# Optimization experiments

Measured on AMD Instinct MI355X. Metric: run time of the kernel, lower is better.

Reference implementation:

```python
import jax, jax.numpy as jnp
import numpy as np

D_MODEL = 768
D_FF = 3072
N_EXPERTS = 4
BATCH, SEQ = 8, 2048


def setup_inputs() -> dict:
    key = jax.random.key(0)
    ks = jax.random.split(key, 8)
    s_in = 1.0 / np.sqrt(D_MODEL)
    s_ff = 1.0 / np.sqrt(D_FF)
    return {
        "hidden_states": jax.random.normal(ks[0], (BATCH, SEQ, D_MODEL), jnp.float32),
        "Wg": jax.random.normal(ks[1], (D_MODEL, N_EXPERTS), jnp.float32) * s_in,
        "bg": jnp.zeros((N_EXPERTS,), jnp.float32),
        "W1": jax.random.normal(ks[2], (N_EXPERTS, D_MODEL, D_FF), jnp.float32) * s_in,
        "b1": jnp.zeros((N_EXPERTS, D_FF), jnp.float32),
        "W2": jax.random.normal(ks[3], (N_EXPERTS, D_FF, D_MODEL), jnp.float32) * s_ff,
        "b2": jnp.zeros((N_EXPERTS, D_MODEL), jnp.float32),
    }


def reference(hidden_states, Wg, bg, W1, b1, W2, b2):
    """Switch-Transformer top-1 MoE FFN (no token dropping).

    router: softmax(x @ Wg + bg); each token goes to argmax expert,
    expert FFN: gelu(x @ W1[e] + b1[e]) @ W2[e] + b2[e],
    output scaled by the winning route probability.
    """
    B, S, D = hidden_states.shape
    xt = hidden_states.reshape(-1, D)                      # [T, D]
    logits = xt @ Wg + bg                                  # [T, E]
    probs = jax.nn.softmax(logits, axis=-1)
    gate = jnp.max(probs, axis=-1)                         # [T]
    route = jnp.argmax(probs, axis=-1)                     # [T] int

    out = jnp.zeros_like(xt)
    for e in range(W1.shape[0]):                           # small fixed expert count
        mask = (route == e).astype(xt.dtype)[:, None]      # [T, 1]
        h = jax.nn.gelu(xt @ W1[e] + b1[e])                # [T, d_ff]
        y = h @ W2[e] + b2[e]                              # [T, D]
        out = out + mask * y
    out = out * gate[:, None]
    return out.reshape(B, S, D)
```

## Files before the change

### kernel.cpp

```cpp
#include <hip/hip_runtime.h>
#include <hip/hip_bf16.h>

#define T_TOK 16384
#define DMODEL 768
#define DFF 3072
#define NEXP 4
#define ROWPAD 512
#define BK 64
#define MBLK_MAX (T_TOK / 128 + NEXP)

typedef __attribute__((ext_vector_type(8))) short bf16x8;
typedef __attribute__((ext_vector_type(4))) float f32x4;

__device__ __forceinline__ void gl_lds16(const void* g, void* l) {
  __builtin_amdgcn_global_load_lds(
      (const __attribute__((address_space(1))) unsigned int*)g,
      (__attribute__((address_space(3))) unsigned int*)l, 16, 0, 0);
}

__device__ __forceinline__ short f2bf(float f) {
  union { float f; unsigned u; } v; v.f = f;
  unsigned r = v.u + 0x7fff + ((v.u >> 16) & 1);
  return (short)(r >> 16);
}

__device__ __forceinline__ float gelu_f(float x) {
  const float c = 0.7978845608028654f;
  float z = c * (x + 0.044715f * x * x * x);
  z = fminf(fmaxf(z, -15.f), 15.f);
  float e = __expf(-2.f * z);
  return 0.5f * x * (1.f + (1.f - e) / (1.f + e));
}


__device__ __forceinline__ int expert_aoff(const int* counts, int e) {
  int off = 0;
  for (int i = 0; i < e; ++i) off += (counts[i] + 127) & ~127;
  return off;
}

__global__ void route_kernel(const float* __restrict__ x, const float* __restrict__ Wg,
                             const float* __restrict__ bg, int* __restrict__ route,
                             float* __restrict__ gate) {
  int t = blockIdx.x * 4 + (threadIdx.x >> 6);
  int l = threadIdx.x & 63;
  const float* xr = x + (size_t)t * DMODEL;
  float s0 = 0.f, s1 = 0.f, s2 = 0.f, s3 = 0.f;
#pragma unroll
  for (int i = 0; i < DMODEL / 64; ++i) {
    int d = l + i * 64;
    float xv = xr[d];
    float4 w = *((const float4*)Wg + d);
    s0 += xv * w.x; s1 += xv * w.y; s2 += xv * w.z; s3 += xv * w.w;
  }
#pragma unroll
  for (int off = 32; off; off >>= 1) {
    s0 += __shfl_xor(s0, off);
    s1 += __shfl_xor(s1, off);
    s2 += __shfl_xor(s2, off);
    s3 += __shfl_xor(s3, off);
  }
  if (l == 0) {
    float lg[4] = { s0 + bg[0], s1 + bg[1], s2 + bg[2], s3 + bg[3] };
    int best = 0; float m = lg[0];
#pragma unroll
    for (int e = 1; e < 4; ++e) if (lg[e] > m) { m = lg[e]; best = e; }
    float s = 0.f;
#pragma unroll
    for (int e = 0; e < 4; ++e) s += __expf(lg[e] - m);
    route[t] = best;
    gate[t] = 1.0f / s;
  }
}

__global__ void bucket_kernel(const int* __restrict__ route, int* __restrict__ counts,
                              int* __restrict__ perm) {
  __shared__ int wcnt[4][NEXP];
  __shared__ int wpre[4][NEXP];
  __shared__ int base[NEXP];
  int tid = threadIdx.x;
  int t = blockIdx.x * 256 + tid;
  int w = tid >> 6, l = tid & 63;
  int r = route[t];
  int lanepre = 0;
  unsigned long long lower = (l == 0) ? 0ull : (~0ull >> (64 - l));
#pragma unroll
  for (int e = 0; e < NEXP; ++e) {
    unsigned long long m = __ballot(r == e);
    if (l == 0) wcnt[w][e] = (int)__popcll(m);
    if (r == e) lanepre = (int)__popcll(m & lower);
  }
  __syncthreads();
  if (tid < NEXP) {
    int s = 0;
#pragma unroll
    for (int ww = 0; ww < 4; ++ww) { wpre[ww][tid] = s; s += wcnt[ww][tid]; }
    base[tid] = atomicAdd(&counts[tid], s);
  }
  __syncthreads();
  int pos = base[r] + wpre[w][r] + lanepre;
  perm[r * T_TOK + pos] = t;
}

__global__ void gather_kernel(const float* __restrict__ x, const int* __restrict__ counts,
                              const int* __restrict__ perm, const float* __restrict__ gate,
                              short* __restrict__ xg, int* __restrict__ tokg,
                              float* __restrict__ gateg) {
  int e = blockIdx.y;
  int cnt = counts[e];
  int pos = blockIdx.x * 8 + (threadIdx.x >> 5);
  if (pos >= cnt) return;
  int off = expert_aoff(counts, e);
  int t = perm[e * T_TOK + pos];
  int g = off + pos;
  int l = threadIdx.x & 31;
  const float* src = x + (size_t)t * DMODEL;
  short* dst = xg + (size_t)g * DMODEL;
  int sw = g & 7;
#pragma unroll
  for (int i = 0; i < 3; ++i) {
    int c = l + 32 * i;
    float4 a = *((const float4*)src + c * 2);
    float4 b = *((const float4*)src + c * 2 + 1);
    bf16x8 v;
    v[0] = f2bf(a.x); v[1] = f2bf(a.y); v[2] = f2bf(a.z); v[3] = f2bf(a.w);
    v[4] = f2bf(b.x); v[5] = f2bf(b.y); v[6] = f2bf(b.z); v[7] = f2bf(b.w);
    int cs = (c & ~7) | ((c & 7) ^ sw);
    *(bf16x8*)(dst + cs * 8) = v;
  }
  if (l == 0) { tokg[g] = t; gateg[g] = gate[t]; }
}

__global__ void transpose_kernel(const float* __restrict__ src, short* __restrict__ dst,
                                 int K, int N) {
  __shared__ float lds[64 * 65];
  int e = blockIdx.z;
  int k0 = blockIdx.x * 64, n0 = blockIdx.y * 64;
  const float* s = src + (size_t)e * K * N;
  short* d = dst + (size_t)e * N * K;
#pragma unroll
  for (int i = 0; i < 16; ++i) {
    int idx = threadIdx.x + i * 256;
    int kk = idx >> 6, nn = idx & 63;
    lds[kk * 65 + nn] = s[(size_t)(k0 + kk) * N + n0 + nn];
  }
  __syncthreads();
#pragma unroll
  for (int i = 0; i < 2; ++i) {
    int cid = threadIdx.x + i * 256;
    int nn = cid >> 3, uu = cid & 7;
    int n = n0 + nn;
    bf16x8 v;
#pragma unroll
    for (int j = 0; j < 8; ++j) v[j] = f2bf(lds[(uu * 8 + j) * 65 + nn]);
    int cs = (k0 >> 3) + (uu ^ (n & 7));
    *(bf16x8*)(d + (size_t)n * K + cs * 8) = v;
  }
}

__global__ void transpose_tiled_kernel(const float* __restrict__ src, short* __restrict__ dst,
                                       int K, int N) {
  __shared__ float lds[64 * 65];
  int e = blockIdx.z;
  int k0 = blockIdx.x * 64, n0 = blockIdx.y * 64;
  const float* s = src + (size_t)e * K * N;
#pragma unroll
  for (int i = 0; i < 16; ++i) {
    int idx = threadIdx.x + i * 256;
    int kk = idx >> 6, nn = idx & 63;
    lds[kk * 65 + nn] = s[(size_t)(k0 + kk) * N + n0 + nn];
  }
  __syncthreads();
  size_t tile = ((size_t)e * (K >> 6) + (k0 >> 6)) * (N >> 6) + (n0 >> 6);
  short* d = dst + tile * 4096;
#pragma unroll
  for (int i = 0; i < 2; ++i) {
    int cid = threadIdx.x + i * 256;
    int nn = cid >> 3, uu = cid & 7;
    int n = n0 + nn;
    bf16x8 v;
#pragma unroll
    for (int j = 0; j < 8; ++j) v[j] = f2bf(lds[(uu * 8 + j) * 65 + nn]);
    int cs = uu ^ (n & 7);
    *(bf16x8*)(d + nn * 64 + cs * 8) = v;
  }
}

__device__ __forceinline__ int xcd_chunk(int orig, int nwg) {
  int q = nwg >> 3, r = nwg & 7, xcd = orig & 7;
  return (xcd < r ? xcd * (q + 1) : r * (q + 1) + (xcd - r) * q) + (orig >> 3);
}

__device__ __forceinline__ bool decode_expert(const int* counts, int gm,
                                              int& e, int& off, int& cnt, int& m0) {
  int c0 = counts[0], c1 = counts[1], c2 = counts[2], c3 = counts[3];
  int mb0 = (c0 + 127) >> 7, mb1 = (c1 + 127) >> 7, mb2 = (c2 + 127) >> 7, mb3 = (c3 + 127) >> 7;
  int o1 = (c0 + 127) & ~127, o2 = o1 + ((c1 + 127) & ~127), o3 = o2 + ((c2 + 127) & ~127);
  if (gm < mb0)                        { e = 0; off = 0;  cnt = c0; m0 = gm << 7; return true; }
  if (gm < mb0 + mb1)                  { e = 1; off = o1; cnt = c1; m0 = (gm - mb0) << 7; return true; }
  if (gm < mb0 + mb1 + mb2)            { e = 2; off = o2; cnt = c2; m0 = (gm - mb0 - mb1) << 7; return true; }
  if (gm < mb0 + mb1 + mb2 + mb3)      { e = 3; off = o3; cnt = c3; m0 = (gm - mb0 - mb1 - mb2) << 7; return true; }
  return false;
}

__global__ __launch_bounds__(256, 4)
void gemm1_kernel(const short* __restrict__ xg, const short* __restrict__ w1t,
                  const float* __restrict__ b1, const int* __restrict__ counts,
                  short* __restrict__ h, int FFC, int chunk, int MBG) {
  __shared__ __align__(16) short smem[2 * 128 * 64];
  short* sA = smem;
  short* sB = smem + 128 * 64;
  int L = xcd_chunk(blockIdx.x, gridDim.x);
  int np = L / MBG, gm = L - np * MBG;
  int e, off, cnt, m0;
  if (!decode_expert(counts, gm, e, off, cnt, m0)) return;
  int n0c = np * 128;
  int n0g = chunk * FFC + n0c;

  const char* Abase = (const char*)(xg + (size_t)(off + m0) * DMODEL);
  const char* Bbase = (const char*)(w1t + (size_t)e * DFF * DMODEL + (size_t)n0g * DMODEL);

  int tid = threadIdx.x, wid = tid >> 6, lane = tid & 63;
  int wm = wid >> 1, wn = wid & 1;
  int l15 = lane & 15, u4 = lane >> 4;

  f32x4 acc[4][4];
#pragma unroll
  for (int i = 0; i < 4; ++i)
#pragma unroll
    for (int j = 0; j < 4; ++j) acc[i][j] = (f32x4){0.f, 0.f, 0.f, 0.f};

  for (int kt = 0; kt < DMODEL / BK; ++kt) {
    int kb = kt * 128;
#pragma unroll
    for (int r = 0; r < 4; ++r) {
      int o = wid * 1024 + r * 4096 + lane * 16;
      int row = o >> 7, b = o & 127;
      gl_lds16(Abase + (size_t)row * (DMODEL * 2) + kb + b, (char*)sA + wid * 1024 + r * 4096);
      gl_lds16(Bbase + (size_t)row * (DMODEL * 2) + kb + b, (char*)sB + wid * 1024 + r * 4096);
    }
    __syncthreads();
#pragma unroll
    for (int ks = 0; ks < 2; ++ks) {
      int u = ks * 4 + u4;
      int slot8 = (u ^ (l15 & 7)) << 3;
      bf16x8 af[4], bfr[4];
#pragma unroll
      for (int mi = 0; mi < 4; ++mi)
        af[mi] = *(const bf16x8*)&sA[(wm * 64 + mi * 16 + l15) * 64 + slot8];
#pragma unroll
      for (int ni = 0; ni < 4; ++ni)
        bfr[ni] = *(const bf16x8*)&sB[(wn * 64 + ni * 16 + l15) * 64 + slot8];
#pragma unroll
      for (int mi = 0; mi < 4; ++mi)
#pragma unroll
        for (int ni = 0; ni < 4; ++ni)
          acc[mi][ni] = __builtin_amdgcn_mfma_f32_16x16x32_bf16(af[mi], bfr[ni], acc[mi][ni], 0, 0, 0);
    }
    __syncthreads();
  }

  float bbs[4];
#pragma unroll
  for (int ni = 0; ni < 4; ++ni) bbs[ni] = b1[e * DFF + n0g + wn * 64 + ni * 16 + l15];
  short* bounce = smem;
#pragma unroll
  for (int mi = 0; mi < 4; ++mi)
#pragma unroll
    for (int ni = 0; ni < 4; ++ni) {
      f32x4 v = acc[mi][ni];
      int col = wn * 64 + ni * 16 + l15;
      int c = col >> 3;
#pragma unroll
      for (int qq = 0; qq < 4; ++qq) {
        int rl = wm * 64 + mi * 16 + u4 * 4 + qq;
        int swc = (c & ~7) | ((c & 7) ^ (rl & 7));
        bounce[rl * 128 + swc * 8 + (col & 7)] = f2bf(gelu_f(v[qq] + bbs[ni]));
      }
    }
  __syncthreads();
  int mblk = (off + m0) >> 7;
  size_t tb = ((size_t)mblk * (FFC >> 6) + (n0c >> 6)) * 8192;
#pragma unroll
  for (int it = 0; it < 8; ++it) {
    int cc = tid + it * 256;
    int rw = cc >> 4, sl = cc & 15;
    size_t dsto = tb + (size_t)(sl >> 3) * 8192 + rw * 64 + (sl & 7) * 8;
    *(bf16x8*)(h + dsto) = *(const bf16x8*)((char*)bounce + cc * 16);
  }
}

__global__ __launch_bounds__(512, 4)
void gemm2_kernel(const short* __restrict__ h, const short* __restrict__ w2t,
                  const float* __restrict__ b2, const int* __restrict__ counts,
                  const int* __restrict__ tokg, const float* __restrict__ gateg,
                  float* __restrict__ out, int FFC, int chunk, int nchunks, int MBG) {
  __shared__ __align__(16) short sA[128 * 64];
  __shared__ __align__(16) short sB[256 * 64];
  int L = xcd_chunk(blockIdx.x, gridDim.x);
  int np = L / MBG, gm = L - np * MBG;
  int e, off, cnt, m0;
  if (!decode_expert(counts, gm, e, off, cnt, m0)) return;
  int n0 = np * 256;

  int mblk = (off + m0) >> 7;
  const char* Atile = (const char*)(h + (size_t)mblk * (FFC >> 6) * 8192);
  const int N64 = DMODEL >> 6;
  const char* Btile = (const char*)(w2t + (((size_t)e * (DFF >> 6)) * N64 + (np << 2)) * 4096);
  const int ktg0 = chunk * (FFC >> 6);

  int tid = threadIdx.x, wid = tid >> 6, lane = tid & 63;
  int wm = wid >> 2, wn = wid & 3;
  int l15 = lane & 15, u4 = lane >> 4;

  f32x4 acc[4][4];
#pragma unroll
  for (int i = 0; i < 4; ++i)
#pragma unroll
    for (int j = 0; j < 4; ++j) acc[i][j] = (f32x4){0.f, 0.f, 0.f, 0.f};

  for (int kt = 0; kt < FFC / BK; ++kt) {
    const char* at = Atile + (size_t)kt * 16384;
    const char* bt = Btile + (size_t)(ktg0 + kt) * (N64 * 8192);
#pragma unroll
    for (int p = 0; p < 2; ++p) {
      int cc = tid + p * 512;
      gl_lds16(at + cc * 16, (char*)sA + (wid * 64 + p * 512) * 16);
    }
#pragma unroll
    for (int p = 0; p < 4; ++p) {
      int cc = tid + p * 512;
      gl_lds16(bt + cc * 16, (char*)sB + (wid * 64 + p * 512) * 16);
    }
    __syncthreads();
#pragma unroll
    for (int ks = 0; ks < 2; ++ks) {
      int u = ks * 4 + u4;
      int slot8 = (u ^ (l15 & 7)) << 3;
      bf16x8 af[4], bfr[4];
#pragma unroll
      for (int mi = 0; mi < 4; ++mi)
        af[mi] = *(const bf16x8*)&sA[(wm * 64 + mi * 16 + l15) * 64 + slot8];
#pragma unroll
      for (int ni = 0; ni < 4; ++ni)
        bfr[ni] = *(const bf16x8*)&sB[(wn * 64 + ni * 16 + l15) * 64 + slot8];
#pragma unroll
      for (int mi = 0; mi < 4; ++mi)
#pragma unroll
        for (int ni = 0; ni < 4; ++ni)
          acc[mi][ni] = __builtin_amdgcn_mfma_f32_16x16x32_bf16(af[mi], bfr[ni], acc[mi][ni], 0, 0, 0);
    }
    __syncthreads();
  }

#pragma unroll
  for (int ni = 0; ni < 4; ++ni) {
    int colg = n0 + wn * 64 + ni * 16 + l15;
    float bb = b2[e * DMODEL + colg];
#pragma unroll
    for (int mi = 0; mi < 4; ++mi) {
      f32x4 v = acc[mi][ni];
#pragma unroll
      for (int qq = 0; qq < 4; ++qq) {
        int ml = m0 + wm * 64 + mi * 16 + u4 * 4 + qq;
        if (ml < cnt) {
          int g = off + ml;
          float* op = out + (size_t)tokg[g] * DMODEL + colg;
          float pv = v[qq];
          if (chunk == 0 && nchunks > 1) {
            *op = pv;
          } else if (chunk < nchunks - 1) {
            *op += pv;
          } else {
            float prev = (nchunks > 1) ? *op : 0.f;
            *op = (prev + pv + bb) * gateg[g];
          }
        }
      }
    }
  }
}

extern "C" void kernel_launch(void* const* d_in, const int* in_sizes, int n_in,
                              void* d_out, int out_size, void* d_ws, size_t ws_size,
                              hipStream_t stream) {
  (void)in_sizes; (void)n_in; (void)out_size;
  const float* x  = (const float*)d_in[0];
  const float* Wg = (const float*)d_in[1];
  const float* bg = (const float*)d_in[2];
  const float* W1 = (const float*)d_in[3];
  const float* b1 = (const float*)d_in[4];
  const float* W2 = (const float*)d_in[5];
  const float* b2 = (const float*)d_in[6];
  float* out = (float*)d_out;
  char* ws = (char*)d_ws;

  size_t cur = 0;
  auto take = [&](size_t bytes) -> size_t {
    cur = (cur + 255) & ~(size_t)255;
    size_t r = cur; cur += bytes; return r;
  };
  size_t o_counts = take(64);
  size_t o_perm  = take((size_t)NEXP * T_TOK * 4);
  size_t o_route = take((size_t)T_TOK * 4);
  size_t o_gate  = take((size_t)T_TOK * 4);
  size_t o_tokg  = take((size_t)(T_TOK + ROWPAD) * 4);
  size_t o_gateg = take((size_t)(T_TOK + ROWPAD) * 4);
  size_t o_w1t   = take((size_t)NEXP * DFF * DMODEL * 2);
  size_t o_w2t   = take((size_t)NEXP * DMODEL * DFF * 2);
  size_t o_xg    = take((size_t)(T_TOK + ROWPAD) * DMODEL * 2);
  cur = (cur + 255) & ~(size_t)255;
  size_t o_h = cur;

  int FFC = 384;
  const int cands[4] = {3072, 1536, 768, 384};
  for (int i = 0; i < 4; ++i) {
    size_t hbytes = (size_t)MBLK_MAX * (cands[i] >> 6) * 16384;
    if (o_h + hbytes <= ws_size) { FFC = cands[i]; break; }
  }

  int*   counts = (int*)(ws + o_counts);
  int*   perm   = (int*)(ws + o_perm);
  int*   routeb = (int*)(ws + o_route);
  float* gate   = (float*)(ws + o_gate);
  int*   tokg   = (int*)(ws + o_tokg);
  float* gateg  = (float*)(ws + o_gateg);
  short* w1t    = (short*)(ws + o_w1t);
  short* w2t    = (short*)(ws + o_w2t);
  short* xg     = (short*)(ws + o_xg);
  short* hbuf   = (short*)(ws + o_h);

  hipMemsetAsync(counts, 0, 64, stream);
  route_kernel<<<T_TOK / 4, 256, 0, stream>>>(x, Wg, bg, routeb, gate);
  bucket_kernel<<<T_TOK / 256, 256, 0, stream>>>(routeb, counts, perm);
  transpose_kernel<<<dim3(DMODEL / 64, DFF / 64, NEXP), 256, 0, stream>>>(W1, w1t, DMODEL, DFF);
  transpose_tiled_kernel<<<dim3(DFF / 64, DMODEL / 64, NEXP), 256, 0, stream>>>(W2, w2t, DFF, DMODEL);
  gather_kernel<<<dim3(T_TOK / 8, NEXP), 256, 0, stream>>>(x, counts, perm, gate, xg, tokg, gateg);

  int NC = DFF / FFC;
  int MBG = T_TOK / 128 + (NEXP - 1);
  int NB2 = DMODEL / 256;
  for (int c = 0; c < NC; ++c) {
    int NB1 = FFC / 128;
    gemm1_kernel<<<NB1 * MBG, 256, 0, stream>>>(xg, w1t, b1, counts, hbuf, FFC, c, MBG);
    gemm2_kernel<<<NB2 * MBG, 512, 0, stream>>>(hbuf, w2t, b2, counts, tokg, gateg, out, FFC, c, NC, MBG);
  }
}
```

Baseline: 274.7 us.

## Use tiled layouts for gathered activations and W1, widen gemm1 tiles

Gathered tokens and transposed W1 are now stored as contiguous 64x64 (or 128x64) swizzled tiles, so each gemm1 K-step loads whole tiles with fully contiguous global-to-LDS copies. gemm1 moves from 128x128 tiles with 256 threads to 128x256 tiles with 512 threads, and the epilogue writes h tiles linearly. The aim is better coalescing and more reuse of the A tile across a wider N. In exchange, gemm1 uses more LDS per block and fewer blocks fit per CU.

```diff
diff --git a/kernel.cpp b/kernel.cpp
--- a/kernel.cpp
+++ b/kernel.cpp
@@ -5,7 +5,6 @@
 #define DMODEL 768
 #define DFF 3072
 #define NEXP 4
-#define ROWPAD 512
 #define BK 64
 #define MBLK_MAX (T_TOK / 128 + NEXP)
 
@@ -115,7 +114,7 @@
   int g = off + pos;
   int l = threadIdx.x & 31;
   const float* src = x + (size_t)t * DMODEL;
-  short* dst = xg + (size_t)g * DMODEL;
+  size_t rbase = ((size_t)(g >> 7) * (DMODEL >> 6)) * 8192 + (g & 127) * 64;
   int sw = g & 7;
 #pragma unroll
   for (int i = 0; i < 3; ++i) {
@@ -125,37 +124,10 @@
     bf16x8 v;
     v[0] = f2bf(a.x); v[1] = f2bf(a.y); v[2] = f2bf(a.z); v[3] = f2bf(a.w);
     v[4] = f2bf(b.x); v[5] = f2bf(b.y); v[6] = f2bf(b.z); v[7] = f2bf(b.w);
-    int cs = (c & ~7) | ((c & 7) ^ sw);
-    *(bf16x8*)(dst + cs * 8) = v;
+    int kt = c >> 3, u = c & 7;
+    *(bf16x8*)(xg + rbase + (size_t)kt * 8192 + ((u ^ sw) << 3)) = v;
   }
   if (l == 0) { tokg[g] = t; gateg[g] = gate[t]; }
-}
-
-__global__ void transpose_kernel(const float* __restrict__ src, short* __restrict__ dst,
-                                 int K, int N) {
-  __shared__ float lds[64 * 65];
-  int e = blockIdx.z;
-  int k0 = blockIdx.x * 64, n0 = blockIdx.y * 64;
-  const float* s = src + (size_t)e * K * N;
-  short* d = dst + (size_t)e * N * K;
-#pragma unroll
-  for (int i = 0; i < 16; ++i) {
-    int idx = threadIdx.x + i * 256;
-    int kk = idx >> 6, nn = idx & 63;
-    lds[kk * 65 + nn] = s[(size_t)(k0 + kk) * N + n0 + nn];
-  }
-  __syncthreads();
-#pragma unroll
-  for (int i = 0; i < 2; ++i) {
-    int cid = threadIdx.x + i * 256;
-    int nn = cid >> 3, uu = cid & 7;
-    int n = n0 + nn;
-    bf16x8 v;
-#pragma unroll
-    for (int j = 0; j < 8; ++j) v[j] = f2bf(lds[(uu * 8 + j) * 65 + nn]);
-    int cs = (k0 >> 3) + (uu ^ (n & 7));
-    *(bf16x8*)(d + (size_t)n * K + cs * 8) = v;
-  }
 }
 
 __global__ void transpose_tiled_kernel(const float* __restrict__ src, short* __restrict__ dst,
@@ -203,25 +175,28 @@
   return false;
 }
 
-__global__ __launch_bounds__(256, 4)
+__global__ __launch_bounds__(512, 2)
 void gemm1_kernel(const short* __restrict__ xg, const short* __restrict__ w1t,
                   const float* __restrict__ b1, const int* __restrict__ counts,
                   short* __restrict__ h, int FFC, int chunk, int MBG) {
-  __shared__ __align__(16) short smem[2 * 128 * 64];
+  __shared__ __align__(16) short smem[32768];
   short* sA = smem;
-  short* sB = smem + 128 * 64;
+  short* sB = smem + 8192;
   int L = xcd_chunk(blockIdx.x, gridDim.x);
   int np = L / MBG, gm = L - np * MBG;
   int e, off, cnt, m0;
   if (!decode_expert(counts, gm, e, off, cnt, m0)) return;
-  int n0c = np * 128;
+  (void)cnt;
+  int n0c = np * 256;
   int n0g = chunk * FFC + n0c;
 
-  const char* Abase = (const char*)(xg + (size_t)(off + m0) * DMODEL);
-  const char* Bbase = (const char*)(w1t + (size_t)e * DFF * DMODEL + (size_t)n0g * DMODEL);
+  int mblk = (off + m0) >> 7;
+  const char* Atile = (const char*)(xg + (size_t)mblk * (DMODEL >> 6) * 8192);
+  const int NB = DFF >> 6;
+  const char* Btile = (const char*)(w1t + (((size_t)e * (DMODEL >> 6)) * NB + (n0g >> 6)) * 4096);
 
   int tid = threadIdx.x, wid = tid >> 6, lane = tid & 63;
-  int wm = wid >> 1, wn = wid & 1;
+  int wm = wid >> 2, wn = wid & 3;
   int l15 = lane & 15, u4 = lane >> 4;
 
   f32x4 acc[4][4];
@@ -231,13 +206,17 @@
     for (int j = 0; j < 4; ++j) acc[i][j] = (f32x4){0.f, 0.f, 0.f, 0.f};
 
   for (int kt = 0; kt < DMODEL / BK; ++kt) {
-    int kb = kt * 128;
-#pragma unroll
-    for (int r = 0; r < 4; ++r) {
-      int o = wid * 1024 + r * 4096 + lane * 16;
-      int row = o >> 7, b = o & 127;
-      gl_lds16(Abase + (size_t)row * (DMODEL * 2) + kb + b, (char*)sA + wid * 1024 + r * 4096);
-      gl_lds16(Bbase + (size_t)row * (DMODEL * 2) + kb + b, (char*)sB + wid * 1024 + r * 4096);
+    const char* at = Atile + (size_t)kt * 16384;
+    const char* bt = Btile + (size_t)kt * (NB * 8192);
+#pragma unroll
+    for (int p = 0; p < 2; ++p) {
+      int cc = tid + p * 512;
+      gl_lds16(at + cc * 16, (char*)sA + (wid * 64 + p * 512) * 16);
+    }
+#pragma unroll
+    for (int p = 0; p < 4; ++p) {
+      int cc = tid + p * 512;
+      gl_lds16(bt + cc * 16, (char*)sB + (wid * 64 + p * 512) * 16);
     }
     __syncthreads();
 #pragma unroll
@@ -263,30 +242,27 @@
   float bbs[4];
 #pragma unroll
   for (int ni = 0; ni < 4; ++ni) bbs[ni] = b1[e * DFF + n0g + wn * 64 + ni * 16 + l15];
-  short* bounce = smem;
 #pragma unroll
   for (int mi = 0; mi < 4; ++mi)
 #pragma unroll
     for (int ni = 0; ni < 4; ++ni) {
       f32x4 v = acc[mi][ni];
       int col = wn * 64 + ni * 16 + l15;
-      int c = col >> 3;
+      int tl = col >> 6, wc = col & 63;
+      int u = wc >> 3, o7 = wc & 7;
 #pragma unroll
       for (int qq = 0; qq < 4; ++qq) {
         int rl = wm * 64 + mi * 16 + u4 * 4 + qq;
-        int swc = (c & ~7) | ((c & 7) ^ (rl & 7));
-        bounce[rl * 128 + swc * 8 + (col & 7)] = f2bf(gelu_f(v[qq] + bbs[ni]));
+        int cs = u ^ (rl & 7);
+        smem[tl * 8192 + rl * 64 + cs * 8 + o7] = f2bf(gelu_f(v[qq] + bbs[ni]));
       }
     }
   __syncthreads();
-  int mblk = (off + m0) >> 7;
   size_t tb = ((size_t)mblk * (FFC >> 6) + (n0c >> 6)) * 8192;
 #pragma unroll
   for (int it = 0; it < 8; ++it) {
-    int cc = tid + it * 256;
-    int rw = cc >> 4, sl = cc & 15;
-    size_t dsto = tb + (size_t)(sl >> 3) * 8192 + rw * 64 + (sl & 7) * 8;
-    *(bf16x8*)(h + dsto) = *(const bf16x8*)((char*)bounce + cc * 16);
+    int cc = tid + it * 512;
+    *(bf16x8*)(h + tb + cc * 8) = *(const bf16x8*)(smem + cc * 8);
   }
 }
 
@@ -404,16 +380,16 @@
   size_t o_perm  = take((size_t)NEXP * T_TOK * 4);
   size_t o_route = take((size_t)T_TOK * 4);
   size_t o_gate  = take((size_t)T_TOK * 4);
-  size_t o_tokg  = take((size_t)(T_TOK + ROWPAD) * 4);
-  size_t o_gateg = take((size_t)(T_TOK + ROWPAD) * 4);
-  size_t o_w1t   = take((size_t)NEXP * DFF * DMODEL * 2);
-  size_t o_w2t   = take((size_t)NEXP * DMODEL * DFF * 2);
-  size_t o_xg    = take((size_t)(T_TOK + ROWPAD) * DMODEL * 2);
+  size_t o_tokg  = take((size_t)(T_TOK + 512) * 4);
+  size_t o_gateg = take((size_t)(T_TOK + 512) * 4);
+  size_t o_w1t   = take((size_t)NEXP * (DMODEL / 64) * (DFF / 64) * 4096 * 2);
+  size_t o_w2t   = take((size_t)NEXP * (DFF / 64) * (DMODEL / 64) * 4096 * 2);
+  size_t o_xg    = take((size_t)MBLK_MAX * (DMODEL / 64) * 8192 * 2);
   cur = (cur + 255) & ~(size_t)255;
   size_t o_h = cur;
 
-  int FFC = 384;
-  const int cands[4] = {3072, 1536, 768, 384};
+  int FFC = 256;
+  const int cands[4] = {3072, 1536, 768, 256};
   for (int i = 0; i < 4; ++i) {
     size_t hbytes = (size_t)MBLK_MAX * (cands[i] >> 6) * 16384;
     if (o_h + hbytes <= ws_size) { FFC = cands[i]; break; }
@@ -433,7 +409,7 @@
   hipMemsetAsync(counts, 0, 64, stream);
   route_kernel<<<T_TOK / 4, 256, 0, stream>>>(x, Wg, bg, routeb, gate);
   bucket_kernel<<<T_TOK / 256, 256, 0, stream>>>(routeb, counts, perm);
-  transpose_kernel<<<dim3(DMODEL / 64, DFF / 64, NEXP), 256, 0, stream>>>(W1, w1t, DMODEL, DFF);
+  transpose_tiled_kernel<<<dim3(DMODEL / 64, DFF / 64, NEXP), 256, 0, stream>>>(W1, w1t, DMODEL, DFF);
   transpose_tiled_kernel<<<dim3(DFF / 64, DMODEL / 64, NEXP), 256, 0, stream>>>(W2, w2t, DFF, DMODEL);
   gather_kernel<<<dim3(T_TOK / 8, NEXP), 256, 0, stream>>>(x, counts, perm, gate, xg, tokg, gateg);
 
@@ -441,8 +417,8 @@
   int MBG = T_TOK / 128 + (NEXP - 1);
   int NB2 = DMODEL / 256;
   for (int c = 0; c < NC; ++c) {
-    int NB1 = FFC / 128;
-    gemm1_kernel<<<NB1 * MBG, 256, 0, stream>>>(xg, w1t, b1, counts, hbuf, FFC, c, MBG);
+    int NB1 = FFC / 256;
+    gemm1_kernel<<<NB1 * MBG, 512, 0, stream>>>(xg, w1t, b1, counts, hbuf, FFC, c, MBG);
     gemm2_kernel<<<NB2 * MBG, 512, 0, stream>>>(hbuf, w2t, b2, counts, tokg, gateg, out, FFC, c, NC, MBG);
   }
 }
```

New measurement: 288.3 us. +4.9%, slower.
